# Kernel optimization log

Measured on AMD Instinct MI355X. Metric: run time of the kernel, lower is better.

## Reference

```python
import jax, jax.numpy as jnp
import numpy as np

N_NODES = 50000
N_EDGES = 800000
IN_FEATS = 9
H_FEATS = 64
HEADS = 3
N_CLASSES = 2
NEG_SLOPE = 0.2  # DGL GATConv default leaky_relu slope


def _gat_layer(x, src, dst, W, attn_l, attn_r, bias, n_nodes):
    """One DGL-style GATConv: returns [N, H, F_out] (pre head-sum)."""
    H, Fo = attn_l.shape
    feat = (x @ W).reshape(n_nodes, H, Fo)            # [N,H,Fo]
    el = jnp.einsum('nhf,hf->nh', feat, attn_l)        # [N,H]
    er = jnp.einsum('nhf,hf->nh', feat, attn_r)        # [N,H]
    e = jax.nn.leaky_relu(el[src] + er[dst], negative_slope=NEG_SLOPE)  # [E,H]
    # edge softmax over incoming edges per destination node
    m = jax.ops.segment_max(e, dst, num_segments=n_nodes)               # [N,H]
    ex = jnp.exp(e - m[dst])                                             # [E,H]
    s = jax.ops.segment_sum(ex, dst, num_segments=n_nodes)              # [N,H]
    alpha = ex / s[dst]                                                  # [E,H]
    # attention-weighted neighbor aggregation
    rst = jax.ops.segment_sum(alpha[:, :, None] * feat[src], dst,
                              num_segments=n_nodes)                      # [N,H,Fo]
    return rst + bias.reshape(1, H, Fo)


def setup_inputs() -> dict:
    key = jax.random.key(0)
    ks = jax.random.split(key, 16)
    feats = jax.random.normal(ks[0], (N_NODES, IN_FEATS), dtype=jnp.float32)
    src = jax.random.randint(ks[1], (N_EDGES,), 0, N_NODES, dtype=jnp.int32)
    dst = jax.random.randint(ks[2], (N_EDGES,), 0, N_NODES, dtype=jnp.int32)
    sc = 0.1
    # layer 1: in_feats -> H*H_FEATS
    W1 = jax.random.normal(ks[3], (IN_FEATS, HEADS * H_FEATS), dtype=jnp.float32) * sc
    al1 = jax.random.normal(ks[4], (HEADS, H_FEATS), dtype=jnp.float32) * sc
    ar1 = jax.random.normal(ks[5], (HEADS, H_FEATS), dtype=jnp.float32) * sc
    b1 = jnp.zeros((HEADS * H_FEATS,), dtype=jnp.float32)
    # middle block layer: H_FEATS -> H*H_FEATS
    W2 = jax.random.normal(ks[6], (H_FEATS, HEADS * H_FEATS), dtype=jnp.float32) * sc
    al2 = jax.random.normal(ks[7], (HEADS, H_FEATS), dtype=jnp.float32) * sc
    ar2 = jax.random.normal(ks[8], (HEADS, H_FEATS), dtype=jnp.float32) * sc
    b2 = jnp.zeros((HEADS * H_FEATS,), dtype=jnp.float32)
    # output layer: H_FEATS -> H*N_CLASSES
    W3 = jax.random.normal(ks[9], (H_FEATS, HEADS * N_CLASSES), dtype=jnp.float32) * sc
    al3 = jax.random.normal(ks[10], (HEADS, N_CLASSES), dtype=jnp.float32) * sc
    ar3 = jax.random.normal(ks[11], (HEADS, N_CLASSES), dtype=jnp.float32) * sc
    b3 = jnp.zeros((HEADS * N_CLASSES,), dtype=jnp.float32)
    return {"feats": feats, "src": src, "dst": dst,
            "W1": W1, "al1": al1, "ar1": ar1, "b1": b1,
            "W2": W2, "al2": al2, "ar2": ar2, "b2": b2,
            "W3": W3, "al3": al3, "ar3": ar3, "b3": b3}


def reference(feats, src, dst, W1, al1, ar1, b1, W2, al2, ar2, b2, W3, al3, ar3, b3):
    # dropout layers are identity at inference (in_dropout/feat_drop skipped)
    h = _gat_layer(feats, src, dst, W1, al1, ar1, b1, N_NODES).sum(axis=1)  # [N,H_FEATS]
    h = _gat_layer(h, src, dst, W2, al2, ar2, b2, N_NODES).sum(axis=1)       # [N,H_FEATS]
    o = _gat_layer(h, src, dst, W3, al3, ar3, b3, N_NODES).sum(axis=1)       # [N,N_CLASSES]
    return o
```

## Files before the change

kernel.cpp:

```cpp
#include <hip/hip_runtime.h>
#include <hip/hip_fp16.h>

#define N_NODES 50000
#define N_EDGES 800000
#define NBKT 196
#define BCAP 4480
#define EPB_BIN 4096
#define NB_BIN ((N_EDGES + EPB_BIN - 1) / EPB_BIN)
#define NB_EL 196
#define NB_PW 48

typedef _Float16 half8 __attribute__((ext_vector_type(8)));
typedef float f32x4 __attribute__((ext_vector_type(4)));

static __device__ __forceinline__ float lrelu(float x) { return fmaxf(x, 0.2f * x); }

static __device__ __forceinline__ float2 h2f(float bits) {
    union { float f; __half2 h; } u;
    u.f = bits;
    return __half22float2(u.h);
}
static __device__ __forceinline__ float f2h2(float a, float b) {
    union { float f; __half2 h; } u;
    u.h = __floats2half2_rn(a, b);
    return u.f;
}

__global__ void __launch_bounds__(256) k_front(const int* __restrict__ src,
                                               const int* __restrict__ dst,
                                               int* __restrict__ bfill,
                                               unsigned int* __restrict__ stage,
                                               const float* __restrict__ x,
                                               const float* __restrict__ W1,
                                               const float* __restrict__ al1,
                                               const float* __restrict__ ar1,
                                               float* __restrict__ xph,
                                               float* __restrict__ er,
                                               const float* __restrict__ W2,
                                               __half* __restrict__ Wt16,
                                               const float* __restrict__ al2,
                                               const float* __restrict__ ar2,
                                               float* __restrict__ Wa2,
                                               float* __restrict__ Wr2) {
    __shared__ int lcnt[NBKT];
    __shared__ int gb[NBKT];
    __shared__ int lf[NBKT];
    __shared__ float sWa[9 * 3];
    __shared__ float sWr[9 * 3];
    const int t = threadIdx.x;
    const int b = blockIdx.x;

    if (b < NB_BIN) {
        const int e0 = b * EPB_BIN;
        for (int i = t; i < NBKT; i += 256) lcnt[i] = 0;
        __syncthreads();
        int dcache[16];
#pragma unroll
        for (int i = 0; i < 16; ++i) {
            const int e = e0 + i * 256 + t;
            if (e < N_EDGES) {
                const int d = dst[e];
                dcache[i] = d;
                atomicAdd(&lcnt[d >> 8], 1);
            } else dcache[i] = -1;
        }
        __syncthreads();
        for (int i = t; i < NBKT; i += 256) {
            gb[i] = i * BCAP + atomicAdd(&bfill[i], lcnt[i]);
            lf[i] = 0;
        }
        __syncthreads();
#pragma unroll
        for (int i = 0; i < 16; ++i) {
            const int e = e0 + i * 256 + t;
            if (e < N_EDGES) {
                const int d = dcache[i];
                const int bk = d >> 8;
                const int r = atomicAdd(&lf[bk], 1);
                stage[gb[bk] + r] = (unsigned int)src[e] | ((unsigned int)(d & 255) << 16);
            }
        }
        return;
    }
    if (b < NB_BIN + NB_EL) {
        if (t < 27) {
            const int h = t / 9, k = t % 9;
            float sa = 0.f, sr = 0.f;
            for (int f = 0; f < 64; ++f) {
                const float w = W1[k * 192 + h * 64 + f];
                sa += w * al1[h * 64 + f];
                sr += w * ar1[h * 64 + f];
            }
            sWa[k * 3 + h] = sa;
            sWr[k * 3 + h] = sr;
        }
        __syncthreads();
        const int n = (b - NB_BIN) * 256 + t;
        if (n >= N_NODES) return;
        const float* __restrict__ xr = x + (size_t)n * 9;
        float xv[9];
        float a0 = 0.f, a1 = 0.f, a2 = 0.f, r0 = 0.f, r1 = 0.f, r2 = 0.f;
#pragma unroll
        for (int k = 0; k < 9; ++k) {
            xv[k] = xr[k];
            a0 += xv[k] * sWa[k * 3 + 0];
            a1 += xv[k] * sWa[k * 3 + 1];
            a2 += xv[k] * sWa[k * 3 + 2];
            r0 += xv[k] * sWr[k * 3 + 0];
            r1 += xv[k] * sWr[k * 3 + 1];
            r2 += xv[k] * sWr[k * 3 + 2];
        }
        float* __restrict__ xo = xph + (size_t)n * 8;
        *reinterpret_cast<float4*>(xo) = make_float4(a0, a1, a2, f2h2(xv[0], xv[1]));
        *reinterpret_cast<float4*>(xo + 4) =
            make_float4(f2h2(xv[2], xv[3]), f2h2(xv[4], xv[5]),
                        f2h2(xv[6], xv[7]), f2h2(xv[8], 0.f));
        *reinterpret_cast<float4*>(er + (size_t)n * 4) = make_float4(r0, r1, r2, 0.f);
        return;
    }
    if (b < NB_BIN + NB_EL + NB_PW) {
        const int idx = (b - (NB_BIN + NB_EL)) * 256 + t;
        if (idx < 64 * 192) {
            const int n = idx / 192, ke = idx % 192;
            Wt16[idx] = __float2half(W2[(ke & 63) * 192 + (ke >> 6) * 64 + n]);
        }
        return;
    }
    if (t < 192) {
        const int h = t >> 6, k = t & 63;
        float sa = 0.f, sr = 0.f;
        for (int f = 0; f < 64; ++f) {
            const float w = W2[k * 192 + h * 64 + f];
            sa += w * al2[h * 64 + f];
            sr += w * ar2[h * 64 + f];
        }
        Wa2[k * 4 + h] = sa;
        Wr2[k * 4 + h] = sr;
        if (h == 0) { Wa2[k * 4 + 3] = 0.f; Wr2[k * 4 + 3] = 0.f; }
    }
}

__global__ void __launch_bounds__(512) k_bscatter2(const unsigned int* __restrict__ stage,
                                                   const int* __restrict__ bfill,
                                                   int* __restrict__ rowp,
                                                   int* __restrict__ col) {
    __shared__ int lcnt[256];
    __shared__ int lpos[256];
    __shared__ int sexc[256];
    __shared__ int sscan[256];
    const int t = threadIdx.x;
    const int b = blockIdx.x;
    const int n0 = b << 8;
    int bv = 0;
    if (t < 256) {
        bv = (t < NBKT) ? bfill[t] : 0;
        sscan[t] = bv;
        lcnt[t] = 0;
    }
    __syncthreads();
    for (int off = 1; off < 256; off <<= 1) {
        int u = 0;
        if (t < 256 && t >= off) u = sscan[t - off];
        __syncthreads();
        if (t < 256) sscan[t] += u;
        __syncthreads();
    }
    const int base = (b == 0) ? 0 : sscan[b - 1];
    const int cnt = bfill[b];
    const unsigned int* __restrict__ st = stage + (size_t)b * BCAP;

    for (int j = t; j < cnt; j += 512)
        atomicAdd(&lcnt[(st[j] >> 16) & 255], 1);
    __syncthreads();
    int v = 0;
    if (t < 256) { v = lcnt[t]; lpos[t] = v; }
    __syncthreads();
    for (int off = 1; off < 256; off <<= 1) {
        int u = 0;
        if (t < 256 && t >= off) u = lpos[t - off];
        __syncthreads();
        if (t < 256) lpos[t] += u;
        __syncthreads();
    }
    if (t < 256) {
        sexc[t] = lpos[t] - v;
        if (n0 + t < N_NODES) rowp[n0 + t] = base + sexc[t];
        lcnt[t] = 0;
    }
    if (b == NBKT - 1 && t == 0) rowp[N_NODES] = N_EDGES;
    __syncthreads();
    for (int j = t; j < cnt; j += 512) {
        const unsigned int e = st[j];
        const int local = (int)(e >> 16) & 255;
        const int r = atomicAdd(&lcnt[local], 1);
        col[base + sexc[local] + r] = (int)(e & 0xFFFFu);
    }
}

__global__ void __launch_bounds__(256, 6) k_l1(const float* __restrict__ xph,
                                               const float* __restrict__ er_in,
                                               const int* __restrict__ rowp,
                                               const int* __restrict__ col,
                                               const float* __restrict__ W1,
                                               const float* __restrict__ b1,
                                               const float* __restrict__ Wa2,
                                               const float* __restrict__ Wr2,
                                               __half* __restrict__ hout,
                                               float* __restrict__ el,
                                               float* __restrict__ er_out) {
    __shared__ union {
        float At[16 * 28];
        float vbuf[16][72];
    } u;
    __shared__ float part[3][16][64];
    const int t = threadIdx.x;
    const int wv = t >> 6;
    const int lane = t & 63;
    const int q = lane >> 4;
    const int ql = lane & 15;
    const int li = wv * 4 + q;
    const int nbase = blockIdx.x * 16;
    const int n = nbase + li;
    const char* __restrict__ xb = (const char*)xph;

    {
        const int jb = rowp[n], je = rowp[n + 1];
        const float4 er4 = *reinterpret_cast<const float4*>(er_in + (size_t)n * 4);
        float acc[27];
#pragma unroll
        for (int j = 0; j < 27; ++j) acc[j] = 0.f;
        float sw0 = 0.f, sw1 = 0.f, sw2 = 0.f;

        for (int e = jb + ql; e < je; e += 32) {
            const int e2 = e + 16;
            const bool v2 = (e2 < je);
            const int off1 = col[e] << 5;
            const int off2 = (v2 ? col[e2] : col[e]) << 5;
            const float4 xa1 = *reinterpret_cast<const float4*>(xb + off1);
            const float4 xb1 = *reinterpret_cast<const float4*>(xb + off1 + 16);
            const float4 xa2 = *reinterpret_cast<const float4*>(xb + off2);
            const float4 xb2 = *reinterpret_cast<const float4*>(xb + off2 + 16);
            const float m2 = v2 ? 1.f : 0.f;
            const float w10 = __expf(lrelu(xa1.x + er4.x));
            const float w11 = __expf(lrelu(xa1.y + er4.y));
            const float w12 = __expf(lrelu(xa1.z + er4.z));
            const float w20 = __expf(lrelu(xa2.x + er4.x)) * m2;
            const float w21 = __expf(lrelu(xa2.y + er4.y)) * m2;
            const float w22 = __expf(lrelu(xa2.z + er4.z)) * m2;
            sw0 += w10 + w20; sw1 += w11 + w21; sw2 += w12 + w22;
            const float2 p10 = h2f(xa1.w), p11 = h2f(xb1.x), p12 = h2f(xb1.y),
                         p13 = h2f(xb1.z), p14 = h2f(xb1.w);
            const float2 p20 = h2f(xa2.w), p21 = h2f(xb2.x), p22 = h2f(xb2.y),
                         p23 = h2f(xb2.z), p24 = h2f(xb2.w);
            const float x1[9] = {p10.x, p10.y, p11.x, p11.y, p12.x, p12.y, p13.x, p13.y, p14.x};
            const float x2[9] = {p20.x, p20.y, p21.x, p21.y, p22.x, p22.y, p23.x, p23.y, p24.x};
#pragma unroll
            for (int k = 0; k < 9; ++k) {
                acc[0 + k]  += w10 * x1[k] + w20 * x2[k];
                acc[9 + k]  += w11 * x1[k] + w21 * x2[k];
                acc[18 + k] += w12 * x1[k] + w22 * x2[k];
            }
        }
#pragma unroll
        for (int off = 1; off < 16; off <<= 1) {
            sw0 += __shfl_xor(sw0, off);
            sw1 += __shfl_xor(sw1, off);
            sw2 += __shfl_xor(sw2, off);
#pragma unroll
            for (int j = 0; j < 27; ++j) acc[j] += __shfl_xor(acc[j], off);
        }
        if (ql == 0) {
            const bool has = (je > jb);
            const float i0 = has ? 1.f / sw0 : 0.f;
            const float i1 = has ? 1.f / sw1 : 0.f;
            const float i2 = has ? 1.f / sw2 : 0.f;
            float* __restrict__ ao = u.At + li * 28;
#pragma unroll
            for (int k = 0; k < 9; ++k) {
                ao[k] = acc[k] * i0;
                ao[9 + k] = acc[9 + k] * i1;
                ao[18 + k] = acc[18 + k] * i2;
            }
        }
    }
    __syncthreads();

    {
        const int h = wv;
        const int c = lane;
        if (h < 3) {
            float wreg[9];
#pragma unroll
            for (int k = 0; k < 9; ++k) wreg[k] = W1[k * 192 + h * 64 + c];
#pragma unroll
            for (int i = 0; i < 16; ++i) {
                const float* __restrict__ arp = u.At + i * 28 + h * 9;
                float acc = 0.f;
#pragma unroll
                for (int k = 0; k < 9; ++k) acc += arp[k] * wreg[k];
                part[h][i][c] = acc;
            }
        }
        __syncthreads();
        const float bsum = b1[c] + b1[64 + c] + b1[128 + c];
        for (int idx = t; idx < 1024; idx += 256) {
            const int i = idx >> 6, cc = idx & 63;
            const float v = part[0][i][cc] + part[1][i][cc] + part[2][i][cc] + bsum;
            hout[(size_t)(nbase + i) * 64 + cc] = __float2half(v);
            u.vbuf[i][cc] = v;
        }
        __syncthreads();
        if (t < 96) {
            const int i = t / 6, r = t % 6;
            const int h3 = (r < 3) ? r : r - 3;
            const float* __restrict__ tab = (r < 3) ? Wa2 : Wr2;
            float s = 0.f;
#pragma unroll 8
            for (int c2 = 0; c2 < 64; ++c2) s += u.vbuf[i][c2] * tab[c2 * 4 + h3];
            if (r < 3) el[(size_t)(nbase + i) * 4 + h3] = s;
            else       er_out[(size_t)(nbase + i) * 4 + h3] = s;
        }
    }
}

__global__ void __launch_bounds__(256, 6) k_aggw64(const __half* __restrict__ x,
                                                   const float* __restrict__ el,
                                                   const float* __restrict__ er,
                                                   const int* __restrict__ rowp,
                                                   const int* __restrict__ col,
                                                   __half* __restrict__ agg) {
    const int t = threadIdx.x;
    const int wv = t >> 6;
    const int lane = t & 63;
    const int q = lane >> 4;
    const int ql = lane & 15;
    const int n = (blockIdx.x * 4 + wv) * 4 + q;
    const int jb = rowp[n], je = rowp[n + 1];

    __shared__ float4 wbuf[4][4][16];
    const float4 er4 = *reinterpret_cast<const float4*>(er + (size_t)n * 4);
    const char* __restrict__ xbase = (const char*)x;
    const char* __restrict__ elbase = (const char*)el;
    const int foff = ql * 8;

    float acc[12];
#pragma unroll
    for (int j = 0; j < 12; ++j) acc[j] = 0.f;
    float sw0 = 0.f, sw1 = 0.f, sw2 = 0.f;

    for (int c0 = jb; c0 < je; c0 += 16) {
        const int cnt = min(16, je - c0);
        if (ql < cnt) {
            const int s = col[c0 + ql];
            const float4 e4 = *reinterpret_cast<const float4*>(elbase + (s << 4));
            const float w0 = __expf(lrelu(e4.x + er4.x));
            const float w1 = __expf(lrelu(e4.y + er4.y));
            const float w2 = __expf(lrelu(e4.z + er4.z));
            wbuf[wv][q][ql] = make_float4(w0, w1, w2, __int_as_float(s << 7));
            sw0 += w0; sw1 += w1; sw2 += w2;
        }
        __builtin_amdgcn_wave_barrier();
        int k = 0;
        for (; k + 4 <= cnt; k += 4) {
            const float4 q0 = wbuf[wv][q][k];
            const float4 q1 = wbuf[wv][q][k + 1];
            const float4 q2 = wbuf[wv][q][k + 2];
            const float4 q3 = wbuf[wv][q][k + 3];
            const float2 r0 = *reinterpret_cast<const float2*>(xbase + (__float_as_int(q0.w) + foff));
            const float2 r1 = *reinterpret_cast<const float2*>(xbase + (__float_as_int(q1.w) + foff));
            const float2 r2 = *reinterpret_cast<const float2*>(xbase + (__float_as_int(q2.w) + foff));
            const float2 r3 = *reinterpret_cast<const float2*>(xbase + (__float_as_int(q3.w) + foff));
            const float2 a01 = h2f(r0.x), a23 = h2f(r0.y);
            const float2 b01 = h2f(r1.x), b23 = h2f(r1.y);
            const float2 c01 = h2f(r2.x), c23 = h2f(r2.y);
            const float2 d01 = h2f(r3.x), d23 = h2f(r3.y);
            acc[0] += q0.x * a01.x + q1.x * b01.x + q2.x * c01.x + q3.x * d01.x;
            acc[1] += q0.x * a01.y + q1.x * b01.y + q2.x * c01.y + q3.x * d01.y;
            acc[2] += q0.x * a23.x + q1.x * b23.x + q2.x * c23.x + q3.x * d23.x;
            acc[3] += q0.x * a23.y + q1.x * b23.y + q2.x * c23.y + q3.x * d23.y;
            acc[4] += q0.y * a01.x + q1.y * b01.x + q2.y * c01.x + q3.y * d01.x;
            acc[5] += q0.y * a01.y + q1.y * b01.y + q2.y * c01.y + q3.y * d01.y;
            acc[6] += q0.y * a23.x + q1.y * b23.x + q2.y * c23.x + q3.y * d23.x;
            acc[7] += q0.y * a23.y + q1.y * b23.y + q2.y * c23.y + q3.y * d23.y;
            acc[8]  += q0.z * a01.x + q1.z * b01.x + q2.z * c01.x + q3.z * d01.x;
            acc[9]  += q0.z * a01.y + q1.z * b01.y + q2.z * c01.y + q3.z * d01.y;
            acc[10] += q0.z * a23.x + q1.z * b23.x + q2.z * c23.x + q3.z * d23.x;
            acc[11] += q0.z * a23.y + q1.z * b23.y + q2.z * c23.y + q3.z * d23.y;
        }
        for (; k < cnt; ++k) {
            const float4 q0 = wbuf[wv][q][k];
            const float2 r0 = *reinterpret_cast<const float2*>(xbase + (__float_as_int(q0.w) + foff));
            const float2 a01 = h2f(r0.x), a23 = h2f(r0.y);
            acc[0] += q0.x * a01.x; acc[1] += q0.x * a01.y;
            acc[2] += q0.x * a23.x; acc[3] += q0.x * a23.y;
            acc[4] += q0.y * a01.x; acc[5] += q0.y * a01.y;
            acc[6] += q0.y * a23.x; acc[7] += q0.y * a23.y;
            acc[8]  += q0.z * a01.x; acc[9]  += q0.z * a01.y;
            acc[10] += q0.z * a23.x; acc[11] += q0.z * a23.y;
        }
    }
#pragma unroll
    for (int off = 1; off < 16; off <<= 1) {
        sw0 += __shfl_xor(sw0, off);
        sw1 += __shfl_xor(sw1, off);
        sw2 += __shfl_xor(sw2, off);
    }
    {
        __half* __restrict__ ao = agg + (size_t)n * 192 + ql * 4;
        if (je > jb) {
            const float i0 = 1.f / sw0, i1 = 1.f / sw1, i2 = 1.f / sw2;
            *reinterpret_cast<float2*>(ao) =
                make_float2(f2h2(acc[0] * i0, acc[1] * i0), f2h2(acc[2] * i0, acc[3] * i0));
            *reinterpret_cast<float2*>(ao + 64) =
                make_float2(f2h2(acc[4] * i1, acc[5] * i1), f2h2(acc[6] * i1, acc[7] * i1));
            *reinterpret_cast<float2*>(ao + 128) =
                make_float2(f2h2(acc[8] * i2, acc[9] * i2), f2h2(acc[10] * i2, acc[11] * i2));
        } else {
            const float2 z = make_float2(f2h2(0.f, 0.f), f2h2(0.f, 0.f));
            *reinterpret_cast<float2*>(ao) = z;
            *reinterpret_cast<float2*>(ao + 64) = z;
            *reinterpret_cast<float2*>(ao + 128) = z;
        }
    }
}

__global__ void __launch_bounds__(256) k_l23(const __half* __restrict__ aggH,
                                             const __half* __restrict__ Wt,
                                             const float* __restrict__ b2,
                                             const float* __restrict__ W3,
                                             const float* __restrict__ al3,
                                             const float* __restrict__ ar3,
                                             float* __restrict__ feat3p,
                                             float* __restrict__ er3) {
    __shared__ float xl[64 * 68];
    __shared__ float Wl[64 * 6];
    __shared__ float Wal[64 * 3];
    __shared__ float Wrl[64 * 3];
    const int t = threadIdx.x;
    const int n0 = blockIdx.x * 64;
    const int nvalid = min(64, N_NODES - n0);

    {
        const int wv = t >> 6;
        const int lane = t & 63;
        const int quad = lane >> 4;
        const int t16 = lane & 15;
        const int nwave = n0 + wv * 16;
        const int arow = min(nwave + t16, N_NODES - 1);
        half8 a[6];
#pragma unroll
        for (int kb = 0; kb < 6; ++kb)
            a[kb] = *reinterpret_cast<const half8*>(aggH + (size_t)arow * 192 + kb * 32 + quad * 8);
#pragma unroll
        for (int nt = 0; nt < 4; ++nt) {
            const int c = nt * 16 + t16;
            const float bs = b2[c] + b2[64 + c] + b2[128 + c];
            const __half* __restrict__ bt = Wt + (size_t)c * 192 + quad * 8;
            f32x4 acc = {0.f, 0.f, 0.f, 0.f};
#pragma unroll
            for (int kb = 0; kb < 6; ++kb) {
                const half8 bfr = *reinterpret_cast<const half8*>(bt + kb * 32);
                acc = __builtin_amdgcn_mfma_f32_16x16x32_f16(a[kb], bfr, acc, 0, 0, 0);
            }
#pragma unroll
            for (int r = 0; r < 4; ++r)
                xl[(wv * 16 + quad * 4 + r) * 68 + c] = acc[r] + bs;
        }
    }
    for (int idx = t; idx < 384; idx += 256) Wl[idx] = W3[idx];
    if (t < 192) {
        const int k = t & 63, h = t >> 6;
        Wal[k * 3 + h] = W3[k * 6 + h * 2] * al3[h * 2] + W3[k * 6 + h * 2 + 1] * al3[h * 2 + 1];
        Wrl[k * 3 + h] = W3[k * 6 + h * 2] * ar3[h * 2] + W3[k * 6 + h * 2 + 1] * ar3[h * 2 + 1];
    }
    __syncthreads();

#pragma unroll
    for (int hp = 0; hp < 2; ++hp) {
        const int i = (t >> 3) + hp * 32;
        const int slot = t & 7;
        if (i < nvalid && slot < 6) {
            float acc = 0.f;
#pragma unroll
            for (int k4 = 0; k4 < 16; ++k4) {
                const float4 xv = *reinterpret_cast<const float4*>(&xl[i * 68 + 4 * k4]);
                acc += Wl[(4 * k4 + 0) * 6 + slot] * xv.x;
                acc += Wl[(4 * k4 + 1) * 6 + slot] * xv.y;
                acc += Wl[(4 * k4 + 2) * 6 + slot] * xv.z;
                acc += Wl[(4 * k4 + 3) * 6 + slot] * xv.w;
            }
            reinterpret_cast<__half*>(feat3p + (size_t)(n0 + i) * 8)[6 + slot] = __float2half(acc);
        }
        if (t < 192) {
            const int ii = t / 6 + hp * 32, ss = t % 6;
            if (ii < nvalid) {
                const int hh = (ss < 3) ? ss : ss - 3;
                const float* __restrict__ wt = (ss < 3) ? Wal : Wrl;
                float acc = 0.f;
#pragma unroll 4
                for (int k = 0; k < 64; ++k) acc += xl[ii * 68 + k] * wt[k * 3 + hh];
                if (ss < 3) feat3p[(size_t)(n0 + ii) * 8 + hh] = acc;
                else        er3[(size_t)(n0 + ii) * 4 + hh] = acc;
            }
        }
    }
}

__global__ void __launch_bounds__(256, 8) k_agg3(const float* __restrict__ feat3p,
                                                 const float* __restrict__ er3,
                                                 const float* __restrict__ b3,
                                                 const int* __restrict__ rowp,
                                                 const int* __restrict__ col,
                                                 float* __restrict__ out) {
    const int t = threadIdx.x;
    const int lane = t & 63;
    const int i16 = lane >> 2;
    const int j = lane & 3;
    const int n = blockIdx.x * 64 + (t >> 6) * 16 + i16;
    const bool valid = (n < N_NODES);
    const int jb = valid ? rowp[n] : 0;
    const int je = valid ? rowp[n + 1] : 0;
    const float4 er4 = valid ? *reinterpret_cast<const float4*>(er3 + (size_t)n * 4)
                             : make_float4(0.f, 0.f, 0.f, 0.f);
    const char* __restrict__ fb = (const char*)feat3p;

    float acc[6];
#pragma unroll
    for (int k = 0; k < 6; ++k) acc[k] = 0.f;
    float sw0 = 0.f, sw1 = 0.f, sw2 = 0.f;

    for (int e = jb + j; e < je; e += 8) {
        const int e2 = e + 4;
        const bool v2 = (e2 < je);
        const int offa = col[e] << 5;
        const int offb = (v2 ? col[e2] : col[e]) << 5;
        const float4 fa1 = *reinterpret_cast<const float4*>(fb + offa);
        const float2 fb1 = *reinterpret_cast<const float2*>(fb + offa + 16);
        const float4 fa2 = *reinterpret_cast<const float4*>(fb + offb);
        const float2 fb2 = *reinterpret_cast<const float2*>(fb + offb + 16);
        const float m2 = v2 ? 1.f : 0.f;
        const float w10 = __expf(lrelu(fa1.x + er4.x));
        const float w11 = __expf(lrelu(fa1.y + er4.y));
        const float w12 = __expf(lrelu(fa1.z + er4.z));
        const float w20 = __expf(lrelu(fa2.x + er4.x)) * m2;
        const float w21 = __expf(lrelu(fa2.y + er4.y)) * m2;
        const float w22 = __expf(lrelu(fa2.z + er4.z)) * m2;
        sw0 += w10 + w20; sw1 += w11 + w21; sw2 += w12 + w22;
        const float2 f01a = h2f(fa1.w), f23a = h2f(fb1.x), f45a = h2f(fb1.y);
        const float2 f01b = h2f(fa2.w), f23b = h2f(fb2.x), f45b = h2f(fb2.y);
        acc[0] += w10 * f01a.x + w20 * f01b.x;
        acc[1] += w10 * f01a.y + w20 * f01b.y;
        acc[2] += w11 * f23a.x + w21 * f23b.x;
        acc[3] += w11 * f23a.y + w21 * f23b.y;
        acc[4] += w12 * f45a.x + w22 * f45b.x;
        acc[5] += w12 * f45a.y + w22 * f45b.y;
    }
#pragma unroll
    for (int off = 1; off < 4; off <<= 1) {
        sw0 += __shfl_xor(sw0, off);
        sw1 += __shfl_xor(sw1, off);
        sw2 += __shfl_xor(sw2, off);
#pragma unroll
        for (int k = 0; k < 6; ++k) acc[k] += __shfl_xor(acc[k], off);
    }
    if (j == 0 && valid) {
        const bool has = (je > jb);
        const float i0 = has ? 1.f / sw0 : 0.f;
        const float i1 = has ? 1.f / sw1 : 0.f;
        const float i2 = has ? 1.f / sw2 : 0.f;
        const float o0 = acc[0] * i0 + acc[2] * i1 + acc[4] * i2 + b3[0] + b3[2] + b3[4];
        const float o1 = acc[1] * i0 + acc[3] * i1 + acc[5] * i2 + b3[1] + b3[3] + b3[5];
        *reinterpret_cast<float2*>(out + (size_t)n * 2) = make_float2(o0, o1);
    }
}

extern "C" void kernel_launch(void* const* d_in, const int* in_sizes, int n_in,
                              void* d_out, int out_size, void* d_ws, size_t ws_size,
                              hipStream_t stream) {
    const float* feats = (const float*)d_in[0];
    const int* src = (const int*)d_in[1];
    const int* dst = (const int*)d_in[2];
    const float* W1 = (const float*)d_in[3];
    const float* al1 = (const float*)d_in[4];
    const float* ar1 = (const float*)d_in[5];
    const float* b1 = (const float*)d_in[6];
    const float* W2 = (const float*)d_in[7];
    const float* al2 = (const float*)d_in[8];
    const float* ar2 = (const float*)d_in[9];
    const float* b2 = (const float*)d_in[10];
    const float* W3 = (const float*)d_in[11];
    const float* al3 = (const float*)d_in[12];
    const float* ar3 = (const float*)d_in[13];
    const float* b3 = (const float*)d_in[14];
    float* out = (float*)d_out;

    char* ws = (char*)d_ws;
    size_t off = 0;
    auto alloc = [&](size_t bytes) {
        void* p = ws + off;
        off += (bytes + 255) & ~(size_t)255;
        return p;
    };
    __half* aggH = (__half*)alloc((size_t)N_NODES * 192 * 2);
    __half* hbufH = (__half*)alloc((size_t)N_NODES * 64 * 2);
    float* xph = (float*)alloc((size_t)N_NODES * 8 * 4);
    float* el = (float*)alloc((size_t)N_NODES * 4 * 4);
    float* er = (float*)alloc((size_t)N_NODES * 4 * 4);
    int* bfill = (int*)alloc(256 * 4);
    int* rowp = (int*)alloc((size_t)(N_NODES + 1) * 4);
    int* col = (int*)alloc((size_t)N_EDGES * 4);
    unsigned int* stage = (unsigned int*)alloc((size_t)NBKT * BCAP * 4);
    __half* Wt16 = (__half*)alloc((size_t)64 * 192 * 2);
    float* Wa2 = (float*)alloc(256 * 4);
    float* Wr2 = (float*)alloc(256 * 4);
    float* feat3p = (float*)alloc((size_t)N_NODES * 8 * 4);
    (void)ws_size;

    const int qb = N_NODES / 16;
    const int nb64 = (N_NODES + 63) / 64;

    hipMemsetAsync(bfill, 0, 256 * 4, stream);
    k_front<<<NB_BIN + NB_EL + NB_PW + 1, 256, 0, stream>>>(
        src, dst, bfill, stage, feats, W1, al1, ar1, xph, er, W2, Wt16,
        al2, ar2, Wa2, Wr2);
    k_bscatter2<<<NBKT, 512, 0, stream>>>(stage, bfill, rowp, col);

    k_l1<<<qb, 256, 0, stream>>>(xph, er, rowp, col, W1, b1, Wa2, Wr2, hbufH, el, er);

    k_aggw64<<<qb, 256, 0, stream>>>(hbufH, el, er, rowp, col, aggH);

    k_l23<<<nb64, 256, 0, stream>>>(aggH, Wt16, b2, W3, al3, ar3, feat3p, er);

    k_agg3<<<nb64, 256, 0, stream>>>(feat3p, er, b3, rowp, col, out);
}
```

Measured before the change: 200.4 us.

## Fuse layer-2 aggregation with MFMA projection and restructure layer-1 gather

Result: faster. 190.1 us (-5.1%).

```diff
diff --git a/kernel.cpp b/kernel.cpp
--- a/kernel.cpp
+++ b/kernel.cpp
@@ -208,6 +208,7 @@
                                                __half* __restrict__ hout,
                                                float* __restrict__ el,
                                                float* __restrict__ er_out) {
+    __shared__ float4 wbuf[4][4][16];
     __shared__ union {
         float At[16 * 28];
         float vbuf[16][72];
@@ -226,39 +227,41 @@
     {
         const int jb = rowp[n], je = rowp[n + 1];
         const float4 er4 = *reinterpret_cast<const float4*>(er_in + (size_t)n * 4);
-        float acc[27];
-#pragma unroll
-        for (int j = 0; j < 27; ++j) acc[j] = 0.f;
+        const int fo = 12 + 2 * (ql < 9 ? ql : 8);
+        float a0 = 0.f, a1 = 0.f, a2 = 0.f;
         float sw0 = 0.f, sw1 = 0.f, sw2 = 0.f;
 
-        for (int e = jb + ql; e < je; e += 32) {
-            const int e2 = e + 16;
-            const bool v2 = (e2 < je);
-            const int off1 = col[e] << 5;
-            const int off2 = (v2 ? col[e2] : col[e]) << 5;
-            const float4 xa1 = *reinterpret_cast<const float4*>(xb + off1);
-            const float4 xb1 = *reinterpret_cast<const float4*>(xb + off1 + 16);
-            const float4 xa2 = *reinterpret_cast<const float4*>(xb + off2);
-            const float4 xb2 = *reinterpret_cast<const float4*>(xb + off2 + 16);
-            const float m2 = v2 ? 1.f : 0.f;
-            const float w10 = __expf(lrelu(xa1.x + er4.x));
-            const float w11 = __expf(lrelu(xa1.y + er4.y));
-            const float w12 = __expf(lrelu(xa1.z + er4.z));
-            const float w20 = __expf(lrelu(xa2.x + er4.x)) * m2;
-            const float w21 = __expf(lrelu(xa2.y + er4.y)) * m2;
-            const float w22 = __expf(lrelu(xa2.z + er4.z)) * m2;
-            sw0 += w10 + w20; sw1 += w11 + w21; sw2 += w12 + w22;
-            const float2 p10 = h2f(xa1.w), p11 = h2f(xb1.x), p12 = h2f(xb1.y),
-                         p13 = h2f(xb1.z), p14 = h2f(xb1.w);
-            const float2 p20 = h2f(xa2.w), p21 = h2f(xb2.x), p22 = h2f(xb2.y),
-                         p23 = h2f(xb2.z), p24 = h2f(xb2.w);
-            const float x1[9] = {p10.x, p10.y, p11.x, p11.y, p12.x, p12.y, p13.x, p13.y, p14.x};
-            const float x2[9] = {p20.x, p20.y, p21.x, p21.y, p22.x, p22.y, p23.x, p23.y, p24.x};
-#pragma unroll
-            for (int k = 0; k < 9; ++k) {
-                acc[0 + k]  += w10 * x1[k] + w20 * x2[k];
-                acc[9 + k]  += w11 * x1[k] + w21 * x2[k];
-                acc[18 + k] += w12 * x1[k] + w22 * x2[k];
+        for (int c0 = jb; c0 < je; c0 += 16) {
+            const int cnt = min(16, je - c0);
+            if (ql < cnt) {
+                const int s = col[c0 + ql];
+                const float4 e4 = *reinterpret_cast<const float4*>(xb + (s << 5));
+                const float w0 = __expf(lrelu(e4.x + er4.x));
+                const float w1 = __expf(lrelu(e4.y + er4.y));
+                const float w2 = __expf(lrelu(e4.z + er4.z));
+                wbuf[wv][q][ql] = make_float4(w0, w1, w2, __int_as_float(s << 5));
+                sw0 += w0; sw1 += w1; sw2 += w2;
+            }
+            __builtin_amdgcn_wave_barrier();
+            int k = 0;
+            for (; k + 2 <= cnt; k += 2) {
+                const float4 q0 = wbuf[wv][q][k];
+                const float4 q1 = wbuf[wv][q][k + 1];
+                const float f0 = __half2float(*reinterpret_cast<const __half*>(
+                    xb + (__float_as_int(q0.w) + fo)));
+                const float f1 = __half2float(*reinterpret_cast<const __half*>(
+                    xb + (__float_as_int(q1.w) + fo)));
+                a0 += q0.x * f0 + q1.x * f1;
+                a1 += q0.y * f0 + q1.y * f1;
+                a2 += q0.z * f0 + q1.z * f1;
+            }
+            if (k < cnt) {
+                const float4 q0 = wbuf[wv][q][k];
+                const float f0 = __half2float(*reinterpret_cast<const __half*>(
+                    xb + (__float_as_int(q0.w) + fo)));
+                a0 += q0.x * f0;
+                a1 += q0.y * f0;
+                a2 += q0.z * f0;
             }
         }
 #pragma unroll
@@ -266,21 +269,16 @@
             sw0 += __shfl_xor(sw0, off);
             sw1 += __shfl_xor(sw1, off);
             sw2 += __shfl_xor(sw2, off);
-#pragma unroll
-            for (int j = 0; j < 27; ++j) acc[j] += __shfl_xor(acc[j], off);
-        }
-        if (ql == 0) {
+        }
+        if (ql < 9) {
             const bool has = (je > jb);
             const float i0 = has ? 1.f / sw0 : 0.f;
             const float i1 = has ? 1.f / sw1 : 0.f;
             const float i2 = has ? 1.f / sw2 : 0.f;
             float* __restrict__ ao = u.At + li * 28;
-#pragma unroll
-            for (int k = 0; k < 9; ++k) {
-                ao[k] = acc[k] * i0;
-                ao[9 + k] = acc[9 + k] * i1;
-                ao[18 + k] = acc[18 + k] * i2;
-            }
+            ao[ql] = a0 * i0;
+            ao[9 + ql] = a1 * i1;
+            ao[18 + ql] = a2 * i2;
         }
     }
     __syncthreads();
@@ -323,90 +321,103 @@
     }
 }
 
-__global__ void __launch_bounds__(256, 6) k_aggw64(const __half* __restrict__ x,
-                                                   const float* __restrict__ el,
-                                                   const float* __restrict__ er,
-                                                   const int* __restrict__ rowp,
-                                                   const int* __restrict__ col,
-                                                   __half* __restrict__ agg) {
+__global__ void __launch_bounds__(256, 6) k_l2(const __half* __restrict__ x,
+                                               const float* __restrict__ el,
+                                               const float* __restrict__ er,
+                                               const int* __restrict__ rowp,
+                                               const int* __restrict__ col,
+                                               const __half* __restrict__ Wt,
+                                               const float* __restrict__ b2,
+                                               const float* __restrict__ W3,
+                                               const float* __restrict__ al3,
+                                               const float* __restrict__ ar3,
+                                               float* __restrict__ feat3p,
+                                               float* __restrict__ er3) {
+    __shared__ float4 wbuf[4][4][16];
+    __shared__ __half aggL[16][200];
+    __shared__ float xl[16 * 68];
+    __shared__ float Wl[384];
+    __shared__ float Wal[192];
+    __shared__ float Wrl[192];
     const int t = threadIdx.x;
     const int wv = t >> 6;
     const int lane = t & 63;
     const int q = lane >> 4;
     const int ql = lane & 15;
-    const int n = (blockIdx.x * 4 + wv) * 4 + q;
-    const int jb = rowp[n], je = rowp[n + 1];
-
-    __shared__ float4 wbuf[4][4][16];
-    const float4 er4 = *reinterpret_cast<const float4*>(er + (size_t)n * 4);
-    const char* __restrict__ xbase = (const char*)x;
-    const char* __restrict__ elbase = (const char*)el;
-    const int foff = ql * 8;
-
-    float acc[12];
-#pragma unroll
-    for (int j = 0; j < 12; ++j) acc[j] = 0.f;
-    float sw0 = 0.f, sw1 = 0.f, sw2 = 0.f;
-
-    for (int c0 = jb; c0 < je; c0 += 16) {
-        const int cnt = min(16, je - c0);
-        if (ql < cnt) {
-            const int s = col[c0 + ql];
-            const float4 e4 = *reinterpret_cast<const float4*>(elbase + (s << 4));
-            const float w0 = __expf(lrelu(e4.x + er4.x));
-            const float w1 = __expf(lrelu(e4.y + er4.y));
-            const float w2 = __expf(lrelu(e4.z + er4.z));
-            wbuf[wv][q][ql] = make_float4(w0, w1, w2, __int_as_float(s << 7));
-            sw0 += w0; sw1 += w1; sw2 += w2;
-        }
-        __builtin_amdgcn_wave_barrier();
-        int k = 0;
-        for (; k + 4 <= cnt; k += 4) {
-            const float4 q0 = wbuf[wv][q][k];
-            const float4 q1 = wbuf[wv][q][k + 1];
-            const float4 q2 = wbuf[wv][q][k + 2];
-            const float4 q3 = wbuf[wv][q][k + 3];
-            const float2 r0 = *reinterpret_cast<const float2*>(xbase + (__float_as_int(q0.w) + foff));
-            const float2 r1 = *reinterpret_cast<const float2*>(xbase + (__float_as_int(q1.w) + foff));
-            const float2 r2 = *reinterpret_cast<const float2*>(xbase + (__float_as_int(q2.w) + foff));
-            const float2 r3 = *reinterpret_cast<const float2*>(xbase + (__float_as_int(q3.w) + foff));
-            const float2 a01 = h2f(r0.x), a23 = h2f(r0.y);
-            const float2 b01 = h2f(r1.x), b23 = h2f(r1.y);
-            const float2 c01 = h2f(r2.x), c23 = h2f(r2.y);
-            const float2 d01 = h2f(r3.x), d23 = h2f(r3.y);
-            acc[0] += q0.x * a01.x + q1.x * b01.x + q2.x * c01.x + q3.x * d01.x;
-            acc[1] += q0.x * a01.y + q1.x * b01.y + q2.x * c01.y + q3.x * d01.y;
-            acc[2] += q0.x * a23.x + q1.x * b23.x + q2.x * c23.x + q3.x * d23.x;
-            acc[3] += q0.x * a23.y + q1.x * b23.y + q2.x * c23.y + q3.x * d23.y;
-            acc[4] += q0.y * a01.x + q1.y * b01.x + q2.y * c01.x + q3.y * d01.x;
-            acc[5] += q0.y * a01.y + q1.y * b01.y + q2.y * c01.y + q3.y * d01.y;
-            acc[6] += q0.y * a23.x + q1.y * b23.x + q2.y * c23.x + q3.y * d23.x;
-            acc[7] += q0.y * a23.y + q1.y * b23.y + q2.y * c23.y + q3.y * d23.y;
-            acc[8]  += q0.z * a01.x + q1.z * b01.x + q2.z * c01.x + q3.z * d01.x;
-            acc[9]  += q0.z * a01.y + q1.z * b01.y + q2.z * c01.y + q3.z * d01.y;
-            acc[10] += q0.z * a23.x + q1.z * b23.x + q2.z * c23.x + q3.z * d23.x;
-            acc[11] += q0.z * a23.y + q1.z * b23.y + q2.z * c23.y + q3.z * d23.y;
-        }
-        for (; k < cnt; ++k) {
-            const float4 q0 = wbuf[wv][q][k];
-            const float2 r0 = *reinterpret_cast<const float2*>(xbase + (__float_as_int(q0.w) + foff));
-            const float2 a01 = h2f(r0.x), a23 = h2f(r0.y);
-            acc[0] += q0.x * a01.x; acc[1] += q0.x * a01.y;
-            acc[2] += q0.x * a23.x; acc[3] += q0.x * a23.y;
-            acc[4] += q0.y * a01.x; acc[5] += q0.y * a01.y;
-            acc[6] += q0.y * a23.x; acc[7] += q0.y * a23.y;
-            acc[8]  += q0.z * a01.x; acc[9]  += q0.z * a01.y;
-            acc[10] += q0.z * a23.x; acc[11] += q0.z * a23.y;
-        }
-    }
-#pragma unroll
-    for (int off = 1; off < 16; off <<= 1) {
-        sw0 += __shfl_xor(sw0, off);
-        sw1 += __shfl_xor(sw1, off);
-        sw2 += __shfl_xor(sw2, off);
-    }
+    const int li = wv * 4 + q;
+    const int nbase = blockIdx.x * 16;
+    const int n = nbase + li;
+
     {
-        __half* __restrict__ ao = agg + (size_t)n * 192 + ql * 4;
+        const int jb = rowp[n], je = rowp[n + 1];
+        const float4 er4 = *reinterpret_cast<const float4*>(er + (size_t)n * 4);
+        const char* __restrict__ xbase = (const char*)x;
+        const char* __restrict__ elbase = (const char*)el;
+        const int foff = ql * 8;
+
+        float acc[12];
+#pragma unroll
+        for (int j = 0; j < 12; ++j) acc[j] = 0.f;
+        float sw0 = 0.f, sw1 = 0.f, sw2 = 0.f;
+
+        for (int c0 = jb; c0 < je; c0 += 16) {
+            const int cnt = min(16, je - c0);
+            if (ql < cnt) {
+                const int s = col[c0 + ql];
+                const float4 e4 = *reinterpret_cast<const float4*>(elbase + (s << 4));
+                const float w0 = __expf(lrelu(e4.x + er4.x));
+                const float w1 = __expf(lrelu(e4.y + er4.y));
+                const float w2 = __expf(lrelu(e4.z + er4.z));
+                wbuf[wv][q][ql] = make_float4(w0, w1, w2, __int_as_float(s << 7));
+                sw0 += w0; sw1 += w1; sw2 += w2;
+            }
+            __builtin_amdgcn_wave_barrier();
+            int k = 0;
+            for (; k + 4 <= cnt; k += 4) {
+                const float4 q0 = wbuf[wv][q][k];
+                const float4 q1 = wbuf[wv][q][k + 1];
+                const float4 q2 = wbuf[wv][q][k + 2];
+                const float4 q3 = wbuf[wv][q][k + 3];
+                const float2 r0 = *reinterpret_cast<const float2*>(xbase + (__float_as_int(q0.w) + foff));
+                const float2 r1 = *reinterpret_cast<const float2*>(xbase + (__float_as_int(q1.w) + foff));
+                const float2 r2 = *reinterpret_cast<const float2*>(xbase + (__float_as_int(q2.w) + foff));
+                const float2 r3 = *reinterpret_cast<const float2*>(xbase + (__float_as_int(q3.w) + foff));
+                const float2 a01 = h2f(r0.x), a23 = h2f(r0.y);
+                const float2 b01 = h2f(r1.x), b23 = h2f(r1.y);
+                const float2 c01 = h2f(r2.x), c23 = h2f(r2.y);
+                const float2 d01 = h2f(r3.x), d23 = h2f(r3.y);
+                acc[0] += q0.x * a01.x + q1.x * b01.x + q2.x * c01.x + q3.x * d01.x;
+                acc[1] += q0.x * a01.y + q1.x * b01.y + q2.x * c01.y + q3.x * d01.y;
+                acc[2] += q0.x * a23.x + q1.x * b23.x + q2.x * c23.x + q3.x * d23.x;
+                acc[3] += q0.x * a23.y + q1.x * b23.y + q2.x * c23.y + q3.x * d23.y;
+                acc[4] += q0.y * a01.x + q1.y * b01.x + q2.y * c01.x + q3.y * d01.x;
+                acc[5] += q0.y * a01.y + q1.y * b01.y + q2.y * c01.y + q3.y * d01.y;
+                acc[6] += q0.y * a23.x + q1.y * b23.x + q2.y * c23.x + q3.y * d23.x;
+                acc[7] += q0.y * a23.y + q1.y * b23.y + q2.y * c23.y + q3.y * d23.y;
+                acc[8]  += q0.z * a01.x + q1.z * b01.x + q2.z * c01.x + q3.z * d01.x;
+                acc[9]  += q0.z * a01.y + q1.z * b01.y + q2.z * c01.y + q3.z * d01.y;
+                acc[10] += q0.z * a23.x + q1.z * b23.x + q2.z * c23.x + q3.z * d23.x;
+                acc[11] += q0.z * a23.y + q1.z * b23.y + q2.z * c23.y + q3.z * d23.y;
+            }
+            for (; k < cnt; ++k) {
+                const float4 q0 = wbuf[wv][q][k];
+                const float2 r0 = *reinterpret_cast<const float2*>(xbase + (__float_as_int(q0.w) + foff));
+                const float2 a01 = h2f(r0.x), a23 = h2f(r0.y);
+                acc[0] += q0.x * a01.x; acc[1] += q0.x * a01.y;
+                acc[2] += q0.x * a23.x; acc[3] += q0.x * a23.y;
+                acc[4] += q0.y * a01.x; acc[5] += q0.y * a01.y;
+                acc[6] += q0.y * a23.x; acc[7] += q0.y * a23.y;
+                acc[8]  += q0.z * a01.x; acc[9]  += q0.z * a01.y;
+                acc[10] += q0.z * a23.x; acc[11] += q0.z * a23.y;
+            }
+        }
+#pragma unroll
+        for (int off = 1; off < 16; off <<= 1) {
+            sw0 += __shfl_xor(sw0, off);
+            sw1 += __shfl_xor(sw1, off);
+            sw2 += __shfl_xor(sw2, off);
+        }
+        __half* __restrict__ ao = &aggL[li][ql * 4];
         if (je > jb) {
             const float i0 = 1.f / sw0, i1 = 1.f / sw1, i2 = 1.f / sw2;
             *reinterpret_cast<float2*>(ao) =
@@ -422,51 +433,6 @@
             *reinterpret_cast<float2*>(ao + 128) = z;
         }
     }
-}
-
-__global__ void __launch_bounds__(256) k_l23(const __half* __restrict__ aggH,
-                                             const __half* __restrict__ Wt,
-                                             const float* __restrict__ b2,
-                                             const float* __restrict__ W3,
-                                             const float* __restrict__ al3,
-                                             const float* __restrict__ ar3,
-                                             float* __restrict__ feat3p,
-                                             float* __restrict__ er3) {
-    __shared__ float xl[64 * 68];
-    __shared__ float Wl[64 * 6];
-    __shared__ float Wal[64 * 3];
-    __shared__ float Wrl[64 * 3];
-    const int t = threadIdx.x;
-    const int n0 = blockIdx.x * 64;
-    const int nvalid = min(64, N_NODES - n0);
-
-    {
-        const int wv = t >> 6;
-        const int lane = t & 63;
-        const int quad = lane >> 4;
-        const int t16 = lane & 15;
-        const int nwave = n0 + wv * 16;
-        const int arow = min(nwave + t16, N_NODES - 1);
-        half8 a[6];
-#pragma unroll
-        for (int kb = 0; kb < 6; ++kb)
-            a[kb] = *reinterpret_cast<const half8*>(aggH + (size_t)arow * 192 + kb * 32 + quad * 8);
-#pragma unroll
-        for (int nt = 0; nt < 4; ++nt) {
-            const int c = nt * 16 + t16;
-            const float bs = b2[c] + b2[64 + c] + b2[128 + c];
-            const __half* __restrict__ bt = Wt + (size_t)c * 192 + quad * 8;
-            f32x4 acc = {0.f, 0.f, 0.f, 0.f};
-#pragma unroll
-            for (int kb = 0; kb < 6; ++kb) {
-                const half8 bfr = *reinterpret_cast<const half8*>(bt + kb * 32);
-                acc = __builtin_amdgcn_mfma_f32_16x16x32_f16(a[kb], bfr, acc, 0, 0, 0);
-            }
-#pragma unroll
-            for (int r = 0; r < 4; ++r)
-                xl[(wv * 16 + quad * 4 + r) * 68 + c] = acc[r] + bs;
-        }
-    }
     for (int idx = t; idx < 384; idx += 256) Wl[idx] = W3[idx];
     if (t < 192) {
         const int k = t & 63, h = t >> 6;
@@ -475,11 +441,32 @@
     }
     __syncthreads();
 
-#pragma unroll
-    for (int hp = 0; hp < 2; ++hp) {
-        const int i = (t >> 3) + hp * 32;
+    {
+        const int quad = lane >> 4;
+        const int t16 = lane & 15;
+        half8 a[6];
+#pragma unroll
+        for (int kb = 0; kb < 6; ++kb)
+            a[kb] = *reinterpret_cast<const half8*>(&aggL[t16][kb * 32 + quad * 8]);
+        const int c = wv * 16 + t16;
+        const float bs = b2[c] + b2[64 + c] + b2[128 + c];
+        const __half* __restrict__ bt = Wt + (size_t)c * 192 + quad * 8;
+        f32x4 acc = {0.f, 0.f, 0.f, 0.f};
+#pragma unroll
+        for (int kb = 0; kb < 6; ++kb) {
+            const half8 bfr = *reinterpret_cast<const half8*>(bt + kb * 32);
+            acc = __builtin_amdgcn_mfma_f32_16x16x32_f16(a[kb], bfr, acc, 0, 0, 0);
+        }
+#pragma unroll
+        for (int r = 0; r < 4; ++r)
+            xl[(quad * 4 + r) * 68 + c] = acc[r] + bs;
+    }
+    __syncthreads();
+
+    if (t < 128) {
+        const int i = t >> 3;
         const int slot = t & 7;
-        if (i < nvalid && slot < 6) {
+        if (slot < 6) {
             float acc = 0.f;
 #pragma unroll
             for (int k4 = 0; k4 < 16; ++k4) {
@@ -489,20 +476,18 @@
                 acc += Wl[(4 * k4 + 2) * 6 + slot] * xv.z;
                 acc += Wl[(4 * k4 + 3) * 6 + slot] * xv.w;
             }
-            reinterpret_cast<__half*>(feat3p + (size_t)(n0 + i) * 8)[6 + slot] = __float2half(acc);
-        }
-        if (t < 192) {
-            const int ii = t / 6 + hp * 32, ss = t % 6;
-            if (ii < nvalid) {
-                const int hh = (ss < 3) ? ss : ss - 3;
-                const float* __restrict__ wt = (ss < 3) ? Wal : Wrl;
-                float acc = 0.f;
+            reinterpret_cast<__half*>(feat3p + (size_t)(nbase + i) * 8)[6 + slot] = __float2half(acc);
+        }
+    } else if (t < 224) {
+        const int tt = t - 128;
+        const int ii = tt / 6, ss = tt % 6;
+        const int hh = (ss < 3) ? ss : ss - 3;
+        const float* __restrict__ wt = (ss < 3) ? Wal : Wrl;
+        float acc = 0.f;
 #pragma unroll 4
-                for (int k = 0; k < 64; ++k) acc += xl[ii * 68 + k] * wt[k * 3 + hh];
-                if (ss < 3) feat3p[(size_t)(n0 + ii) * 8 + hh] = acc;
-                else        er3[(size_t)(n0 + ii) * 4 + hh] = acc;
-            }
-        }
+        for (int k = 0; k < 64; ++k) acc += xl[ii * 68 + k] * wt[k * 3 + hh];
+        if (ss < 3) feat3p[(size_t)(nbase + ii) * 8 + hh] = acc;
+        else        er3[(size_t)(nbase + ii) * 4 + hh] = acc;
     }
 }
 
@@ -601,7 +586,6 @@
         off += (bytes + 255) & ~(size_t)255;
         return p;
     };
-    __half* aggH = (__half*)alloc((size_t)N_NODES * 192 * 2);
     __half* hbufH = (__half*)alloc((size_t)N_NODES * 64 * 2);
     float* xph = (float*)alloc((size_t)N_NODES * 8 * 4);
     float* el = (float*)alloc((size_t)N_NODES * 4 * 4);
@@ -627,9 +611,8 @@
 
     k_l1<<<qb, 256, 0, stream>>>(xph, er, rowp, col, W1, b1, Wa2, Wr2, hbufH, el, er);
 
-    k_aggw64<<<qb, 256, 0, stream>>>(hbufH, el, er, rowp, col, aggH);
-
-    k_l23<<<nb64, 256, 0, stream>>>(aggH, Wt16, b2, W3, al3, ar3, feat3p, er);
+    k_l2<<<qb, 256, 0, stream>>>(hbufH, el, er, rowp, col, Wt16, b2,
+                                 W3, al3, ar3, feat3p, er);
 
     k_agg3<<<nb64, 256, 0, stream>>>(feat3p, er, b3, rowp, col, out);
 }
```
